# Performance work log

Hardware: AMD Instinct MI355X
Metric: run time of the kernel (lower is better)

Reference implementation:

```python
import jax, jax.numpy as jnp
import numpy as np

GAMMA = 267.513e6  # gyromagnetic ratio of 1H, rad/s/T


def setup_inputs() -> dict:
    key = jax.random.key(0)
    k1, k2 = jax.random.split(key, 2)
    N_meas = 64
    g = jax.random.normal(k2, (N_meas, 3), dtype=jnp.float32)
    g = g / jnp.linalg.norm(g, axis=1, keepdims=True)          # unit gradient directions
    G_amps = 0.02 + 0.06 * jax.random.uniform(k1, (N_meas,), dtype=jnp.float32)  # 20-80 mT/m
    return {
        "G_amps": G_amps,
        "gradients": g,
        "D_long": jnp.float32(2.0e-9),    # m^2/s, fiber-parallel diffusivity
        "D_trans": jnp.float32(5.0e-10),  # m^2/s, transverse diffusivity
        "delta_us": 10000,  # gradient pulse duration, microseconds
        "Delta_us": 30000,  # pulse separation, microseconds
        "dt_us": 100,       # SDE step, microseconds
        "N_particles": 50000,
        "seed": 0,
    }


def reference(G_amps, gradients, D_long, D_trans, delta_us, Delta_us, dt_us, N_particles, seed):
    dt = dt_us * 1e-6
    delta = delta_us * 1e-6
    Delta = Delta_us * 1e-6
    T_max = Delta + delta + dt
    times = jnp.arange(0.0, T_max, dt, dtype=jnp.float32)      # (T,)
    T = times.shape[0]

    # --- Euler-Maruyama SDE solve (free anisotropic diffusion, fiber = e_z, k_conf=0) ---
    # per-axis noise scale: sqrt(2 * D * dt), transverse on x/y, longitudinal on z
    sig = jnp.sqrt(2.0 * dt * jnp.stack([D_trans, D_trans, D_long]))  # (3,)
    base_key = jax.random.key(seed)
    y0 = jnp.zeros((N_particles, 3), dtype=jnp.float32)

    def step(y, i):
        n = jax.random.normal(jax.random.fold_in(base_key, i), (N_particles, 3), dtype=jnp.float32)
        y_next = y + sig * n
        return y_next, y_next

    _, rest = jax.lax.scan(step, y0, jnp.arange(T - 1))
    traj = jnp.concatenate([y0[None], rest], axis=0)           # (T, N, 3)

    # --- trapezoidal PGSE gradient envelope (rise time = dt), shared across measurements ---
    rise = dt
    def pulse(t0):
        return (jnp.clip((times - t0) / rise, 0.0, 1.0)
                - jnp.clip((times - t0 - delta) / rise, 0.0, 1.0))
    env = pulse(0.0) - pulse(Delta)                            # (T,)

    # --- phase integration, fused: contract time first to avoid (M,T,N) intermediates ---
    S = jnp.einsum('t,tnd->nd', env, traj)                     # (N, 3) envelope-weighted position sum
    phases = (GAMMA * dt) * jnp.einsum('m,md,nd->mn', G_amps, gradients, S)  # (M, N)
    c = jnp.mean(jnp.cos(phases), axis=1)
    s = jnp.mean(jnp.sin(phases), axis=1)
    return jnp.sqrt(c * c + s * s)                             # |mean exp(i*phase)| per measurement
```

## Files before the change

kernel.cpp:

```cpp
#include <hip/hip_runtime.h>
#include <stdint.h>

#define N_PART  50000
#define HALF_N  25000
#define STEPS   400
#define T_PTS   401
#define CHUNKS  20
#define SPC     (STEPS / CHUNKS)
#define BITS_SPLIT 75000u
#define NSPLIT  8
#define BLK     256

__device__ __forceinline__ void threefry2x32(uint32_t k0, uint32_t k1,
                                             uint32_t x0, uint32_t x1,
                                             uint32_t& o0, uint32_t& o1) {
  const uint32_t ks2 = k0 ^ k1 ^ 0x1BD11BDAu;
  x0 += k0; x1 += k1;
#define RND(r) { x0 += x1; x1 = (x1 << r) | (x1 >> (32 - r)); x1 ^= x0; }
  RND(13) RND(15) RND(26) RND(6)
  x0 += k1;  x1 += ks2 + 1u;
  RND(17) RND(29) RND(16) RND(24)
  x0 += ks2; x1 += k0 + 2u;
  RND(13) RND(15) RND(26) RND(6)
  x0 += k0;  x1 += k1 + 3u;
  RND(17) RND(29) RND(16) RND(24)
  x0 += k1;  x1 += ks2 + 4u;
  RND(13) RND(15) RND(26) RND(6)
  x0 += ks2; x1 += k0 + 5u;
#undef RND
  o0 = x0; o1 = x1;
}

__device__ __forceinline__ float bits_to_erfinv(uint32_t bits) {
  const float lo = __uint_as_float(0xBF7FFFFFu);
  float m = __uint_as_float((bits >> 9) | 0x3F800000u);
  float u = fmaxf(lo, fmaf(m, 2.0f, -3.0f));
  float t = fmaf(-u, u, 1.0f);
  float L = __log2f(t);
  float p;
  if (L > -7.2134752f) {
    float w = fmaf(L, -0.69314718056f, -2.5f);
    p = 2.81022636e-08f;
    p = fmaf(p, w, 3.43273939e-07f);
    p = fmaf(p, w, -3.5233877e-06f);
    p = fmaf(p, w, -4.39150654e-06f);
    p = fmaf(p, w, 0.00021858087f);
    p = fmaf(p, w, -0.00125372503f);
    p = fmaf(p, w, -0.00417768164f);
    p = fmaf(p, w, 0.246640727f);
    p = fmaf(p, w, 1.50140941f);
  } else {
    float w = sqrtf(L * -0.69314718056f) - 3.0f;
    p = -0.000200214257f;
    p = fmaf(p, w, 0.000100950558f);
    p = fmaf(p, w, 0.00134934322f);
    p = fmaf(p, w, -0.00367342844f);
    p = fmaf(p, w, 0.00573950773f);
    p = fmaf(p, w, -0.0076224613f);
    p = fmaf(p, w, 0.00943887047f);
    p = fmaf(p, w, 1.00167406f);
    p = fmaf(p, w, 2.83297682f);
  }
  return p * u;
}

__global__ __launch_bounds__(BLK) void sde_kernel(const float* __restrict__ D_long,
                                                  const float* __restrict__ D_trans,
                                                  const int* __restrict__ delta_us,
                                                  const int* __restrict__ Delta_us,
                                                  const int* __restrict__ dt_us,
                                                  const int* __restrict__ seed,
                                                  float* __restrict__ Sbuf) {
  __shared__ float sA[T_PTS], sB[T_PTS];
  __shared__ uint4 kw[STEPS];
  int tid = threadIdx.x;

  {
    float u  = (float)dt_us[0]    * 1e-6f;
    float df = (float)delta_us[0] * 1e-6f;
    float Df = (float)Delta_us[0] * 1e-6f;
    for (int t = tid; t < T_PTS; t += BLK) {
      float tm = (float)t * u;
      float c1 = fminf(fmaxf(tm / u, 0.0f), 1.0f);
      float c2 = fminf(fmaxf((tm - df) / u, 0.0f), 1.0f);
      float c3 = fminf(fmaxf((tm - Df) / u, 0.0f), 1.0f);
      float c4 = fminf(fmaxf(((tm - Df) - df) / u, 0.0f), 1.0f);
      sA[t] = (c1 - c2) - (c3 - c4);
    }
  }
  __syncthreads();

  {
    float* src = sA; float* dst = sB;
    for (int d = 1; d < T_PTS; d <<= 1) {
      for (int i = tid; i < T_PTS; i += BLK)
        dst[i] = src[i] + ((i + d < T_PTS) ? src[i + d] : 0.0f);
      __syncthreads();
      float* tmp = src; src = dst; dst = tmp;
    }
    uint32_t sd = (uint32_t)seed[0];
    for (int i = tid; i < STEPS; i += BLK) {
      uint32_t o0, o1;
      threefry2x32(0u, sd, 0u, (uint32_t)i, o0, o1);
      kw[i] = make_uint4(o0, o1, __float_as_uint(1.41421356237309515f * src[i + 1]), 0u);
    }
  }
  __syncthreads();

  uint32_t item = blockIdx.x * BLK + tid;
  if (item < CHUNKS * HALF_N) {
    uint32_t chunk = item / HALF_N;
    uint32_t p = item - chunk * HALF_N;
    const uint32_t c0 = 3u * p;
    const int i0 = (int)chunk * SPC;

    float a0x = 0.f, a0y = 0.f, a0z = 0.f;
    float a1x = 0.f, a1y = 0.f, a1z = 0.f;

    for (int s = 0; s < SPC; ++s) {
      uint4 k = kw[i0 + s];
      float w = __uint_as_float(k.z);
      uint32_t o0, o1;
      threefry2x32(k.x, k.y, c0,      c0 + BITS_SPLIT,      o0, o1);
      a0x = fmaf(w, bits_to_erfinv(o0), a0x);
      a1x = fmaf(w, bits_to_erfinv(o1), a1x);
      threefry2x32(k.x, k.y, c0 + 1u, c0 + 1u + BITS_SPLIT, o0, o1);
      a0y = fmaf(w, bits_to_erfinv(o0), a0y);
      a1y = fmaf(w, bits_to_erfinv(o1), a1y);
      threefry2x32(k.x, k.y, c0 + 2u, c0 + 2u + BITS_SPLIT, o0, o1);
      a0z = fmaf(w, bits_to_erfinv(o0), a0z);
      a1z = fmaf(w, bits_to_erfinv(o1), a1z);
    }

    float twodt = 2.0f * ((float)dt_us[0] * 1e-6f);
    float st = sqrtf(twodt * D_trans[0]);
    float sl = sqrtf(twodt * D_long[0]);

    atomicAdd(&Sbuf[3 * p + 0], a0x * st);
    atomicAdd(&Sbuf[3 * p + 1], a0y * st);
    atomicAdd(&Sbuf[3 * p + 2], a0z * sl);
    atomicAdd(&Sbuf[3 * (p + HALF_N) + 0], a1x * st);
    atomicAdd(&Sbuf[3 * (p + HALF_N) + 1], a1y * st);
    atomicAdd(&Sbuf[3 * (p + HALF_N) + 2], a1z * sl);
  }
}

__global__ __launch_bounds__(BLK) void signal_partial(const float* __restrict__ Sbuf,
                                                      const float* __restrict__ G_amps,
                                                      const float* __restrict__ grad,
                                                      const int* __restrict__ dt_us,
                                                      float* __restrict__ acc,
                                                      float* __restrict__ out) {
  int m = blockIdx.x;
  int n0 = blockIdx.y * (N_PART / NSPLIT);
  int tid = threadIdx.x;
  float Kf = 267.513e6f * ((float)dt_us[0] * 1e-6f);
  float Km = Kf * G_amps[m];
  float gx = grad[3 * m + 0], gy = grad[3 * m + 1], gz = grad[3 * m + 2];

  float cs = 0.f, ss = 0.f;
  for (int n = n0 + tid; n < n0 + N_PART / NSPLIT; n += BLK) {
    float sx = Sbuf[3 * n + 0], sy = Sbuf[3 * n + 1], sz = Sbuf[3 * n + 2];
    float ph = Km * (gx * sx + gy * sy + gz * sz);
    float s, c;
    __sincosf(ph, &s, &c);
    cs += c; ss += s;
  }
  for (int off = 32; off > 0; off >>= 1) {
    cs += __shfl_down(cs, off);
    ss += __shfl_down(ss, off);
  }
  __shared__ float redc[4], reds[4];
  __shared__ int slast;
  int lane = tid & 63, wv = tid >> 6;
  if (lane == 0) { redc[wv] = cs; reds[wv] = ss; }
  __syncthreads();
  if (tid == 0) {
    atomicAdd(&acc[m],      redc[0] + redc[1] + redc[2] + redc[3]);
    atomicAdd(&acc[64 + m], reds[0] + reds[1] + reds[2] + reds[3]);
    __threadfence();
    unsigned* ctr = (unsigned*)&acc[128];
    unsigned done = __hip_atomic_fetch_add(ctr, 1u, __ATOMIC_ACQ_REL, __HIP_MEMORY_SCOPE_AGENT);
    slast = (done == (unsigned)(gridDim.x * gridDim.y) - 1u) ? 1 : 0;
  }
  __syncthreads();
  if (slast && tid < (int)gridDim.x) {
    float c = __hip_atomic_load(&acc[tid],      __ATOMIC_RELAXED, __HIP_MEMORY_SCOPE_AGENT) / (float)N_PART;
    float s = __hip_atomic_load(&acc[64 + tid], __ATOMIC_RELAXED, __HIP_MEMORY_SCOPE_AGENT) / (float)N_PART;
    out[tid] = sqrtf(c * c + s * s);
  }
}

extern "C" void kernel_launch(void* const* d_in, const int* in_sizes, int n_in,
                              void* d_out, int out_size, void* d_ws, size_t ws_size,
                              hipStream_t stream) {
  const float* G_amps   = (const float*)d_in[0];
  const float* grad     = (const float*)d_in[1];
  const float* D_long   = (const float*)d_in[2];
  const float* D_trans  = (const float*)d_in[3];
  const int*   delta_us = (const int*)d_in[4];
  const int*   Delta_us = (const int*)d_in[5];
  const int*   dt_us    = (const int*)d_in[6];
  const int*   seed     = (const int*)d_in[8];

  float* Sbuf = (float*)d_ws;
  float* acc  = (float*)((char*)d_ws + 600000);

  hipMemsetAsync(d_ws, 0, 600520, stream);
  int sde_blocks = (CHUNKS * HALF_N + BLK - 1) / BLK;
  sde_kernel<<<sde_blocks, BLK, 0, stream>>>(D_long, D_trans, delta_us, Delta_us,
                                             dt_us, seed, Sbuf);
  int M = in_sizes[0];
  signal_partial<<<dim3(M, NSPLIT), BLK, 0, stream>>>(Sbuf, G_amps, grad, dt_us,
                                                      acc, (float*)d_out);
}
```

Baseline: 176.8 us.

## Reduce SDE time-chunks in shared memory per block instead of global atomics

Reorganizes the SDE kernel so each 320-thread block handles 16 particle pairs across all 20 time chunks, reducing the chunk partial sums through shared memory and writing Sbuf directly rather than with global atomicAdds. This drops the 600KB memset: the accumulator is zeroed inside the first SDE block. It also software-prefetches the next step key in the unrolled loop. The cost is one extra block-wide sync and shared-memory reduction per block, and each block must redo the 400-step key/envelope setup for far fewer particles, since there are about 1563 blocks.

After: 290.1 us. 64.1% more time.

```diff
diff --git a/kernel.cpp b/kernel.cpp
--- a/kernel.cpp
+++ b/kernel.cpp
@@ -9,7 +9,9 @@
 #define SPC     (STEPS / CHUNKS)
 #define BITS_SPLIT 75000u
 #define NSPLIT  8
-#define BLK     256
+#define BLK     320
+#define PAIRS_PER_BLK 16
+#define SDE_BLOCKS ((HALF_N + PAIRS_PER_BLK - 1) / PAIRS_PER_BLK)
 
 __device__ __forceinline__ void threefry2x32(uint32_t k0, uint32_t k1,
                                              uint32_t x0, uint32_t x1,
@@ -70,10 +72,14 @@
                                                   const int* __restrict__ Delta_us,
                                                   const int* __restrict__ dt_us,
                                                   const int* __restrict__ seed,
-                                                  float* __restrict__ Sbuf) {
+                                                  float* __restrict__ Sbuf,
+                                                  float* __restrict__ acc) {
   __shared__ float sA[T_PTS], sB[T_PTS];
-  __shared__ uint4 kw[STEPS];
+  __shared__ uint4 kwls[STEPS];
+  __shared__ float red[CHUNKS * 97];
   int tid = threadIdx.x;
+
+  if (blockIdx.x == 0 && tid < 130) acc[tid] = 0.0f;
 
   {
     float u  = (float)dt_us[0]    * 1e-6f;
@@ -102,50 +108,61 @@
     for (int i = tid; i < STEPS; i += BLK) {
       uint32_t o0, o1;
       threefry2x32(0u, sd, 0u, (uint32_t)i, o0, o1);
-      kw[i] = make_uint4(o0, o1, __float_as_uint(1.41421356237309515f * src[i + 1]), 0u);
-    }
-  }
-  __syncthreads();
-
-  uint32_t item = blockIdx.x * BLK + tid;
-  if (item < CHUNKS * HALF_N) {
-    uint32_t chunk = item / HALF_N;
-    uint32_t p = item - chunk * HALF_N;
-    const uint32_t c0 = 3u * p;
-    const int i0 = (int)chunk * SPC;
-
-    float a0x = 0.f, a0y = 0.f, a0z = 0.f;
-    float a1x = 0.f, a1y = 0.f, a1z = 0.f;
-
-    for (int s = 0; s < SPC; ++s) {
-      uint4 k = kw[i0 + s];
-      float w = __uint_as_float(k.z);
-      uint32_t o0, o1;
-      threefry2x32(k.x, k.y, c0,      c0 + BITS_SPLIT,      o0, o1);
-      a0x = fmaf(w, bits_to_erfinv(o0), a0x);
-      a1x = fmaf(w, bits_to_erfinv(o1), a1x);
-      threefry2x32(k.x, k.y, c0 + 1u, c0 + 1u + BITS_SPLIT, o0, o1);
-      a0y = fmaf(w, bits_to_erfinv(o0), a0y);
-      a1y = fmaf(w, bits_to_erfinv(o1), a1y);
-      threefry2x32(k.x, k.y, c0 + 2u, c0 + 2u + BITS_SPLIT, o0, o1);
-      a0z = fmaf(w, bits_to_erfinv(o0), a0z);
-      a1z = fmaf(w, bits_to_erfinv(o1), a1z);
-    }
-
-    float twodt = 2.0f * ((float)dt_us[0] * 1e-6f);
-    float st = sqrtf(twodt * D_trans[0]);
-    float sl = sqrtf(twodt * D_long[0]);
-
-    atomicAdd(&Sbuf[3 * p + 0], a0x * st);
-    atomicAdd(&Sbuf[3 * p + 1], a0y * st);
-    atomicAdd(&Sbuf[3 * p + 2], a0z * sl);
-    atomicAdd(&Sbuf[3 * (p + HALF_N) + 0], a1x * st);
-    atomicAdd(&Sbuf[3 * (p + HALF_N) + 1], a1y * st);
-    atomicAdd(&Sbuf[3 * (p + HALF_N) + 2], a1z * sl);
-  }
-}
-
-__global__ __launch_bounds__(BLK) void signal_partial(const float* __restrict__ Sbuf,
+      kwls[i] = make_uint4(o0, o1, __float_as_uint(1.41421356237309515f * src[i + 1]), 0u);
+    }
+  }
+  __syncthreads();
+
+  const int pair  = tid & 15;
+  const int chunk = tid >> 4;
+  const uint32_t pg = blockIdx.x * PAIRS_PER_BLK + pair;
+  const uint32_t c0 = 3u * pg;
+  const int i0 = chunk * SPC;
+
+  float a0x = 0.f, a0y = 0.f, a0z = 0.f;
+  float a1x = 0.f, a1y = 0.f, a1z = 0.f;
+
+  uint4 kc = kwls[i0];
+  #pragma unroll
+  for (int s = 0; s < SPC; ++s) {
+    uint4 kn = kwls[i0 + ((s + 1 < SPC) ? s + 1 : s)];
+    float w = __uint_as_float(kc.z);
+    uint32_t o0, o1;
+    threefry2x32(kc.x, kc.y, c0,      c0 + BITS_SPLIT,      o0, o1);
+    a0x = fmaf(w, bits_to_erfinv(o0), a0x);
+    a1x = fmaf(w, bits_to_erfinv(o1), a1x);
+    threefry2x32(kc.x, kc.y, c0 + 1u, c0 + 1u + BITS_SPLIT, o0, o1);
+    a0y = fmaf(w, bits_to_erfinv(o0), a0y);
+    a1y = fmaf(w, bits_to_erfinv(o1), a1y);
+    threefry2x32(kc.x, kc.y, c0 + 2u, c0 + 2u + BITS_SPLIT, o0, o1);
+    a0z = fmaf(w, bits_to_erfinv(o0), a0z);
+    a1z = fmaf(w, bits_to_erfinv(o1), a1z);
+    kc = kn;
+  }
+
+  {
+    int base = chunk * 97 + pair * 6;
+    red[base + 0] = a0x; red[base + 1] = a0y; red[base + 2] = a0z;
+    red[base + 3] = a1x; red[base + 4] = a1y; red[base + 5] = a1z;
+  }
+  __syncthreads();
+  if (tid < PAIRS_PER_BLK * 6) {
+    float sum = 0.0f;
+    #pragma unroll
+    for (int c = 0; c < CHUNKS; ++c) sum += red[c * 97 + tid];
+    int p = tid / 6, comp = tid - 6 * p;
+    uint32_t pg2 = blockIdx.x * PAIRS_PER_BLK + p;
+    if (pg2 < HALF_N) {
+      float twodt = 2.0f * ((float)dt_us[0] * 1e-6f);
+      float sig = sqrtf(twodt * (((comp == 2) | (comp == 5)) ? D_long[0] : D_trans[0]));
+      int axis = (comp < 3) ? comp : comp - 3;
+      uint32_t particle = (comp < 3) ? pg2 : pg2 + HALF_N;
+      Sbuf[3 * particle + axis] = sum * sig;
+    }
+  }
+}
+
+__global__ __launch_bounds__(256) void signal_partial(const float* __restrict__ Sbuf,
                                                       const float* __restrict__ G_amps,
                                                       const float* __restrict__ grad,
                                                       const int* __restrict__ dt_us,
@@ -159,7 +176,7 @@
   float gx = grad[3 * m + 0], gy = grad[3 * m + 1], gz = grad[3 * m + 2];
 
   float cs = 0.f, ss = 0.f;
-  for (int n = n0 + tid; n < n0 + N_PART / NSPLIT; n += BLK) {
+  for (int n = n0 + tid; n < n0 + N_PART / NSPLIT; n += 256) {
     float sx = Sbuf[3 * n + 0], sy = Sbuf[3 * n + 1], sz = Sbuf[3 * n + 2];
     float ph = Km * (gx * sx + gy * sy + gz * sz);
     float s, c;
@@ -206,11 +223,9 @@
   float* Sbuf = (float*)d_ws;
   float* acc  = (float*)((char*)d_ws + 600000);
 
-  hipMemsetAsync(d_ws, 0, 600520, stream);
-  int sde_blocks = (CHUNKS * HALF_N + BLK - 1) / BLK;
-  sde_kernel<<<sde_blocks, BLK, 0, stream>>>(D_long, D_trans, delta_us, Delta_us,
-                                             dt_us, seed, Sbuf);
+  sde_kernel<<<SDE_BLOCKS, BLK, 0, stream>>>(D_long, D_trans, delta_us, Delta_us,
+                                             dt_us, seed, Sbuf, acc);
   int M = in_sizes[0];
-  signal_partial<<<dim3(M, NSPLIT), BLK, 0, stream>>>(Sbuf, G_amps, grad, dt_us,
+  signal_partial<<<dim3(M, NSPLIT), 256, 0, stream>>>(Sbuf, G_amps, grad, dt_us,
                                                       acc, (float*)d_out);
 }
```
